# Kernel tuning notes

Measured on AMD Instinct MI355X. Metric: run time of the kernel, lower is better.

## Reference

```python
import jax, jax.numpy as jnp
import numpy as np

DIM = 768
NUM_HEADS = 12
HEAD_DIM = DIM // NUM_HEADS
SCALE = HEAD_DIM ** -0.5


def setup_inputs() -> dict:
    key = jax.random.key(0)
    k_x, k_qkv, k_proj, k_pb = jax.random.split(key, 4)
    B, N = 8, 1024
    x = jax.random.normal(k_x, (B, N, DIM), dtype=jnp.float32)
    # nn.Linear(dim, 3*dim, bias=False): weight [3*dim, dim]
    w_qkv = jax.random.normal(k_qkv, (3 * DIM, DIM), dtype=jnp.float32) * (DIM ** -0.5)
    # nn.Linear(dim, dim): weight [dim, dim], bias [dim]
    w_proj = jax.random.normal(k_proj, (DIM, DIM), dtype=jnp.float32) * (DIM ** -0.5)
    b_proj = jax.random.normal(k_pb, (DIM,), dtype=jnp.float32) * 0.01
    return {"x": x, "w_qkv": w_qkv, "w_proj": w_proj, "b_proj": b_proj}


def reference(x, w_qkv, w_proj, b_proj):
    B, N, C = x.shape
    H, D = NUM_HEADS, HEAD_DIM
    # qkv: [B, N, 3C] -> [3, B, H, N, D]
    qkv = jnp.einsum('bnc,oc->bno', x, w_qkv)
    qkv = qkv.reshape(B, N, 3, H, D).transpose(2, 0, 3, 1, 4)
    q, k, v = qkv[0], qkv[1], qkv[2]
    # scores in float32 (module explicitly casts to float)
    attn = jnp.einsum('bhnd,bhmd->bhnm', q.astype(jnp.float32), k.astype(jnp.float32)) * SCALE
    attn = jax.nn.softmax(attn, axis=-1)
    attn = jnp.where(jnp.isnan(attn), 0.0, attn)  # masked_fill nan -> 0
    out = jnp.einsum('bhnm,bhmd->bhnd', attn, v.astype(jnp.float32))
    out = out.transpose(0, 2, 1, 3).reshape(B, N, C)
    out = jnp.einsum('bnc,oc->bno', out, w_proj) + b_proj
    return out
```

## Files before the change

### kernel.cpp

```cpp
#include <hip/hip_runtime.h>

typedef _Float16 half8 __attribute__((ext_vector_type(8)));
typedef _Float16 half4 __attribute__((ext_vector_type(4)));
typedef float f32x4 __attribute__((ext_vector_type(4)));

#define NHEAD 12
#define HDIM  64
#define SEQ   1024
#define CDIM  768
#define O3    2304
#define MTOK  8192

__device__ __forceinline__ void load_lds16(const void* g, void* l) {
  __builtin_amdgcn_global_load_lds(
      (const __attribute__((address_space(1))) unsigned int*)g,
      (__attribute__((address_space(3))) unsigned int*)l, 16, 0, 0);
}

__global__ __launch_bounds__(256) void cast_f2h(const float* __restrict__ in,
                                                _Float16* __restrict__ out) {
  size_t i = ((size_t)blockIdx.x * 256 + threadIdx.x) * 4;
  float4 v = *reinterpret_cast<const float4*>(in + i);
  half4 h;
  h[0] = (_Float16)v.x; h[1] = (_Float16)v.y; h[2] = (_Float16)v.z; h[3] = (_Float16)v.w;
  *reinterpret_cast<half4*>(out + i) = h;
}

__global__ __launch_bounds__(256, 4) void qkv_gemm(const _Float16* __restrict__ A,
                                                   const _Float16* __restrict__ Bw,
                                                   _Float16* __restrict__ Qh,
                                                   _Float16* __restrict__ Kh,
                                                   _Float16* __restrict__ VT) {
  __shared__ _Float16 As0[128 * 32], Bs0[128 * 32];
  __shared__ _Float16 As1[128 * 32], Bs1[128 * 32];
  const int tid  = threadIdx.x;
  const int lane = tid & 63;
  const int wv   = tid >> 6;
  const int wm   = wv >> 1;
  const int wn   = wv & 1;
  const int fr   = lane & 15;
  const int kg   = lane >> 4;

  const int lin = blockIdx.y * gridDim.x + blockIdx.x;
  const int k   = lin & 7;
  const int j   = lin >> 3;
  const int n0  = (j >> 3) * 128;
  const int m0  = (k * 8 + (j & 7)) * 128;

  f32x4 acc[4][4];
#pragma unroll
  for (int i = 0; i < 4; ++i)
#pragma unroll
    for (int j2 = 0; j2 < 4; ++j2) acc[i][j2] = (f32x4){0.f, 0.f, 0.f, 0.f};

  auto stage = [&](_Float16* Ad, _Float16* Bd, int kt) {
#pragma unroll
    for (int r = 0; r < 2; ++r) {
      const int c = r * 256 + tid;
      const int row = c >> 2, cc = c & 3;
      load_lds16(A + (size_t)(m0 + row) * CDIM + kt + ((cc ^ (row & 3)) * 8), Ad + c * 8);
    }
#pragma unroll
    for (int r = 0; r < 2; ++r) {
      const int c = r * 256 + tid;
      const int row = c >> 2, cc = c & 3;
      load_lds16(Bw + (size_t)(n0 + row) * CDIM + kt + ((cc ^ (row & 3)) * 8), Bd + c * 8);
    }
  };

  auto compute = [&](const _Float16* As, const _Float16* Bs) {
    half8 a[4], b[4];
#pragma unroll
    for (int i = 0; i < 4; ++i) {
      const int row = wm * 64 + i * 16 + fr;
      a[i] = *reinterpret_cast<const half8*>(&As[row * 32 + ((kg ^ (row & 3)) * 8)]);
    }
#pragma unroll
    for (int j2 = 0; j2 < 4; ++j2) {
      const int row = wn * 64 + j2 * 16 + fr;
      b[j2] = *reinterpret_cast<const half8*>(&Bs[row * 32 + ((kg ^ (row & 3)) * 8)]);
    }
#pragma unroll
    for (int i = 0; i < 4; ++i)
#pragma unroll
      for (int j2 = 0; j2 < 4; ++j2)
        acc[i][j2] = __builtin_amdgcn_mfma_f32_16x16x32_f16(a[i], b[j2], acc[i][j2], 0, 0, 0);
  };

  stage(As0, Bs0, 0);
  __syncthreads();
  for (int it = 0; it < 12; ++it) {
    const int kt = it * 64;
    stage(As1, Bs1, kt + 32);
    compute(As0, Bs0);
    __syncthreads();
    if (kt + 64 < CDIM) stage(As0, Bs0, kt + 64);
    compute(As1, Bs1);
    __syncthreads();
  }

  const float QSCALE = 0.125f * 1.44269504088896f;
  const int t     = n0 / CDIM;
  const int hbase = n0 - t * CDIM;
#pragma unroll
  for (int i = 0; i < 4; ++i) {
    const int mrow = m0 + wm * 64 + i * 16 + kg * 4;
#pragma unroll
    for (int j2 = 0; j2 < 4; ++j2) {
      const int hd = hbase + wn * 64 + j2 * 16 + fr;
      const int h  = hd >> 6, d = hd & 63;
#pragma unroll
      for (int r = 0; r < 4; ++r) {
        const int m  = mrow + r;
        const int bb = m >> 10, nn = m & 1023;
        const float v = acc[i][j2][r];
        if (t == 0)
          Qh[(((size_t)(bb * NHEAD + h)) << 16) + (nn << 6) + d] = (_Float16)(v * QSCALE);
        else if (t == 1)
          Kh[(((size_t)(bb * NHEAD + h)) << 16) + (nn << 6) + d] = (_Float16)v;
        else
          VT[(((size_t)(bb * NHEAD + h)) << 16) + (d << 10) + nn] = (_Float16)v;
      }
    }
  }
}

__global__ __launch_bounds__(512) void attn_kernel(const _Float16* __restrict__ Qh,
                                                   const _Float16* __restrict__ Kh,
                                                   const _Float16* __restrict__ VT,
                                                   _Float16* __restrict__ AO) {
  __shared__ _Float16 Ks0[64 * 64], Vs0[64 * 64];
  __shared__ _Float16 Ks1[64 * 64], Vs1[64 * 64];
  __shared__ _Float16 Ps[8 * 16 * 64];
  const int tid  = threadIdx.x;
  const int lane = tid & 63;
  const int w    = tid >> 6;
  const int fr   = lane & 15;
  const int kg   = lane >> 4;
  const int kh   = kg * 8;
  const int bh   = blockIdx.x;
  const int qt   = blockIdx.y;
  const int q0   = qt * 128 + w * 16;
  const size_t qkbase = (size_t)bh * SEQ * HDIM;
  char* const psw = (char*)&Ps[w * 16 * 64];

  half8 qb[2];
#pragma unroll
  for (int ks = 0; ks < 2; ++ks)
    qb[ks] = *reinterpret_cast<const half8*>(
        &Qh[qkbase + (size_t)(q0 + fr) * HDIM + ks * 32 + kh]);

  f32x4 O[4];
  float mrun = -__builtin_inff();
  float lrun = 0.f;
#pragma unroll
  for (int fd = 0; fd < 4; ++fd) O[fd] = (f32x4){0.f, 0.f, 0.f, 0.f};

  auto stageKV = [&](_Float16* Kd, _Float16* Vd, int kt) {
    const int c = tid;
    const int row = c >> 3, cc = c & 7;
    load_lds16(&Kh[qkbase + (size_t)(kt + row) * HDIM + ((cc ^ (row & 7)) * 8)], Kd + c * 8);
    load_lds16(&VT[(size_t)bh * HDIM * SEQ + (size_t)row * SEQ + kt + ((cc ^ (row & 7)) * 8)],
               Vd + c * 8);
  };

  auto computeKV = [&](const _Float16* Ksrc, const _Float16* Vsrc) {
    f32x4 st[4];
#pragma unroll
    for (int fc = 0; fc < 4; ++fc) st[fc] = (f32x4){0.f, 0.f, 0.f, 0.f};
#pragma unroll
    for (int ks = 0; ks < 2; ++ks) {
#pragma unroll
      for (int fc = 0; fc < 4; ++fc) {
        const int row = fc * 16 + fr;
        const int colh = ks * 32 + kh;
        half8 ka = *reinterpret_cast<const half8*>(
            &Ksrc[row * 64 + (((colh >> 3) ^ (row & 7)) << 3)]);
        st[fc] = __builtin_amdgcn_mfma_f32_16x16x32_f16(ka, qb[ks], st[fc], 0, 0, 0);
      }
    }

    float mx = st[0][0];
#pragma unroll
    for (int fc = 0; fc < 4; ++fc)
#pragma unroll
      for (int r = 0; r < 4; ++r) mx = fmaxf(mx, st[fc][r]);
    mx = fmaxf(mx, __shfl_xor(mx, 16));
    mx = fmaxf(mx, __shfl_xor(mx, 32));

    if (!__all(mx - mrun <= 8.f)) {
      const float mnew = fmaxf(mrun, mx);
      const float corr = exp2f(mrun - mnew);
      mrun = mnew;
      lrun *= corr;
#pragma unroll
      for (int r = 0; r < 4; ++r) {
        const float c4 = __shfl(corr, kg * 4 + r);
#pragma unroll
        for (int fd = 0; fd < 4; ++fd) O[fd][r] *= c4;
      }
    }

    float rs = 0.f;
#pragma unroll
    for (int fc = 0; fc < 4; ++fc)
#pragma unroll
      for (int r = 0; r < 4; ++r) {
        const float p = exp2f(st[fc][r] - mrun);
        st[fc][r] = p;
        rs += p;
      }
    rs += __shfl_xor(rs, 16);
    rs += __shfl_xor(rs, 32);
    lrun += rs;

#pragma unroll
    for (int fc = 0; fc < 4; ++fc) {
      half4 pk;
      pk[0] = (_Float16)st[fc][0];
      pk[1] = (_Float16)st[fc][1];
      pk[2] = (_Float16)st[fc][2];
      pk[3] = (_Float16)st[fc][3];
      const int slot = (fc * 2 + (kg >> 1)) ^ (fr & 7);
      *reinterpret_cast<half4*>(psw + fr * 128 + slot * 16 + (kg & 1) * 8) = pk;
    }

#pragma unroll
    for (int ks = 0; ks < 2; ++ks) {
      const int rslot = (ks * 4 + kg) ^ (fr & 7);
      half8 pa = *reinterpret_cast<half8*>(psw + fr * 128 + rslot * 16);
#pragma unroll
      for (int fd = 0; fd < 4; ++fd) {
        const int row = fd * 16 + fr;
        const int colh = ks * 32 + kh;
        half8 vb = *reinterpret_cast<const half8*>(
            &Vsrc[row * 64 + (((colh >> 3) ^ (row & 7)) << 3)]);
        O[fd] = __builtin_amdgcn_mfma_f32_16x16x32_f16(pa, vb, O[fd], 0, 0, 0);
      }
    }
  };

  stageKV(Ks0, Vs0, 0);
  __syncthreads();
  for (int it = 0; it < 8; ++it) {
    const int kt = it * 128;
    stageKV(Ks1, Vs1, kt + 64);
    computeKV(Ks0, Vs0);
    __syncthreads();
    if (kt + 128 < SEQ) stageKV(Ks0, Vs0, kt + 128);
    computeKV(Ks1, Vs1);
    __syncthreads();
  }

  const int b = bh / NHEAD, h = bh % NHEAD;
  const float linv = 1.0f / lrun;
#pragma unroll
  for (int r = 0; r < 4; ++r) {
    const float lq = __shfl(linv, kg * 4 + r);
    const int n = q0 + kg * 4 + r;
#pragma unroll
    for (int fd = 0; fd < 4; ++fd)
      AO[((size_t)b * SEQ + n) * CDIM + h * HDIM + fd * 16 + fr] =
          (_Float16)(O[fd][r] * lq);
  }
}

__global__ __launch_bounds__(256, 4) void proj_gemm(const _Float16* __restrict__ A,
                                                    const _Float16* __restrict__ Bw,
                                                    const float* __restrict__ bias,
                                                    float* __restrict__ Out) {
  __shared__ _Float16 As0[128 * 32], Bs0[128 * 32];
  __shared__ _Float16 As1[128 * 32], Bs1[128 * 32];
  const int tid  = threadIdx.x;
  const int lane = tid & 63;
  const int wv   = tid >> 6;
  const int wm   = wv >> 1;
  const int wn   = wv & 1;
  const int fr   = lane & 15;
  const int kg   = lane >> 4;

  const int lin = blockIdx.y * gridDim.x + blockIdx.x;
  const int k   = lin & 7;
  const int j   = lin >> 3;
  const int n0  = (j >> 3) * 128;
  const int m0  = (k * 8 + (j & 7)) * 128;

  f32x4 acc[4][4];
#pragma unroll
  for (int i = 0; i < 4; ++i)
#pragma unroll
    for (int j2 = 0; j2 < 4; ++j2) acc[i][j2] = (f32x4){0.f, 0.f, 0.f, 0.f};

  auto stage = [&](_Float16* Ad, _Float16* Bd, int kt) {
#pragma unroll
    for (int r = 0; r < 2; ++r) {
      const int c = r * 256 + tid;
      const int row = c >> 2, cc = c & 3;
      load_lds16(A + (size_t)(m0 + row) * CDIM + kt + ((cc ^ (row & 3)) * 8), Ad + c * 8);
    }
#pragma unroll
    for (int r = 0; r < 2; ++r) {
      const int c = r * 256 + tid;
      const int row = c >> 2, cc = c & 3;
      load_lds16(Bw + (size_t)(n0 + row) * CDIM + kt + ((cc ^ (row & 3)) * 8), Bd + c * 8);
    }
  };

  auto compute = [&](const _Float16* As, const _Float16* Bs) {
    half8 a[4], b[4];
#pragma unroll
    for (int i = 0; i < 4; ++i) {
      const int row = wm * 64 + i * 16 + fr;
      a[i] = *reinterpret_cast<const half8*>(&As[row * 32 + ((kg ^ (row & 3)) * 8)]);
    }
#pragma unroll
    for (int j2 = 0; j2 < 4; ++j2) {
      const int row = wn * 64 + j2 * 16 + fr;
      b[j2] = *reinterpret_cast<const half8*>(&Bs[row * 32 + ((kg ^ (row & 3)) * 8)]);
    }
#pragma unroll
    for (int i = 0; i < 4; ++i)
#pragma unroll
      for (int j2 = 0; j2 < 4; ++j2)
        acc[i][j2] = __builtin_amdgcn_mfma_f32_16x16x32_f16(a[i], b[j2], acc[i][j2], 0, 0, 0);
  };

  stage(As0, Bs0, 0);
  __syncthreads();
  for (int it = 0; it < 12; ++it) {
    const int kt = it * 64;
    stage(As1, Bs1, kt + 32);
    compute(As0, Bs0);
    __syncthreads();
    if (kt + 64 < CDIM) stage(As0, Bs0, kt + 64);
    compute(As1, Bs1);
    __syncthreads();
  }

#pragma unroll
  for (int i = 0; i < 4; ++i) {
    const int mrow = m0 + wm * 64 + i * 16 + kg * 4;
#pragma unroll
    for (int j2 = 0; j2 < 4; ++j2) {
      const int ocol = n0 + wn * 64 + j2 * 16 + fr;
      const float bv = bias[ocol];
#pragma unroll
      for (int r = 0; r < 4; ++r)
        Out[(size_t)(mrow + r) * CDIM + ocol] = acc[i][j2][r] + bv;
    }
  }
}

extern "C" void kernel_launch(void* const* d_in, const int* in_sizes, int n_in,
                              void* d_out, int out_size, void* d_ws, size_t ws_size,
                              hipStream_t stream) {
  const float* x     = (const float*)d_in[0];
  const float* wqkv  = (const float*)d_in[1];
  const float* wproj = (const float*)d_in[2];
  const float* bproj = (const float*)d_in[3];
  float* out = (float*)d_out;

  char* ws = (char*)d_ws;
  _Float16* x_h     = (_Float16*)(ws);
  _Float16* wqkv_h  = (_Float16*)(ws + 12582912);
  _Float16* wproj_h = (_Float16*)(ws + 16121856);
  _Float16* Qh      = (_Float16*)(ws + 17301504);
  _Float16* Kh      = (_Float16*)(ws + 29884416);
  _Float16* VT      = (_Float16*)(ws + 42467328);
  _Float16* AOh     = (_Float16*)(ws + 55050240);

  cast_f2h<<<6291456 / 1024, 256, 0, stream>>>(x, x_h);
  cast_f2h<<<1769472 / 1024, 256, 0, stream>>>(wqkv, wqkv_h);
  cast_f2h<<<589824 / 1024, 256, 0, stream>>>(wproj, wproj_h);

  qkv_gemm<<<dim3(O3 / 128, MTOK / 128), 256, 0, stream>>>(x_h, wqkv_h, Qh, Kh, VT);
  attn_kernel<<<dim3(96, 8), 512, 0, stream>>>(Qh, Kh, VT, AOh);
  proj_gemm<<<dim3(CDIM / 128, MTOK / 128), 256, 0, stream>>>(AOh, wproj_h, bproj, out);
}
```

Measured before the change: 139.1 us.

## Use 4-stage LDS ring with vmcnt waits and stronger swizzle in GEMMs

The QKV and projection GEMMs move from a double buffer with two __syncthreads per 64-wide K step to a 4-slot LDS ring. Loads run two 32-wide K tiles ahead, with one barrier per tile and explicit s_waitcnt vmcnt counts, so global-to-LDS loads overlap MFMA compute. The LDS XOR swizzle also folds in (row>>2)&3 to cut bank conflicts on fragment reads. LDS per block doubles to 64KB and the minimum-occupancy hint of 4 blocks is dropped, which may lower occupancy. The hand-set vmcnt values are fragile if the compiler reorders or adds memory ops.

```diff
diff --git a/kernel.cpp b/kernel.cpp
--- a/kernel.cpp
+++ b/kernel.cpp
@@ -26,13 +26,13 @@
   *reinterpret_cast<half4*>(out + i) = h;
 }
 
-__global__ __launch_bounds__(256, 4) void qkv_gemm(const _Float16* __restrict__ A,
-                                                   const _Float16* __restrict__ Bw,
-                                                   _Float16* __restrict__ Qh,
-                                                   _Float16* __restrict__ Kh,
-                                                   _Float16* __restrict__ VT) {
-  __shared__ _Float16 As0[128 * 32], Bs0[128 * 32];
-  __shared__ _Float16 As1[128 * 32], Bs1[128 * 32];
+__global__ __launch_bounds__(256) void qkv_gemm(const _Float16* __restrict__ A,
+                                                const _Float16* __restrict__ Bw,
+                                                _Float16* __restrict__ Qh,
+                                                _Float16* __restrict__ Kh,
+                                                _Float16* __restrict__ VT) {
+  __shared__ _Float16 AsAll[4][128 * 32];
+  __shared__ _Float16 BsAll[4][128 * 32];
   const int tid  = threadIdx.x;
   const int lane = tid & 63;
   const int wv   = tid >> 6;
@@ -40,6 +40,7 @@
   const int wn   = wv & 1;
   const int fr   = lane & 15;
   const int kg   = lane >> 4;
+  const int kswz = kg ^ (fr & 3) ^ ((fr >> 2) & 3);
 
   const int lin = blockIdx.y * gridDim.x + blockIdx.x;
   const int k   = lin & 7;
@@ -53,18 +54,22 @@
 #pragma unroll
     for (int j2 = 0; j2 < 4; ++j2) acc[i][j2] = (f32x4){0.f, 0.f, 0.f, 0.f};
 
-  auto stage = [&](_Float16* Ad, _Float16* Bd, int kt) {
+  auto stage = [&](int slot, int kt) {
+    _Float16* Ad = AsAll[slot];
+    _Float16* Bd = BsAll[slot];
 #pragma unroll
     for (int r = 0; r < 2; ++r) {
       const int c = r * 256 + tid;
       const int row = c >> 2, cc = c & 3;
-      load_lds16(A + (size_t)(m0 + row) * CDIM + kt + ((cc ^ (row & 3)) * 8), Ad + c * 8);
+      const int g = cc ^ (row & 3) ^ ((row >> 2) & 3);
+      load_lds16(A + (size_t)(m0 + row) * CDIM + kt + g * 8, Ad + c * 8);
     }
 #pragma unroll
     for (int r = 0; r < 2; ++r) {
       const int c = r * 256 + tid;
       const int row = c >> 2, cc = c & 3;
-      load_lds16(Bw + (size_t)(n0 + row) * CDIM + kt + ((cc ^ (row & 3)) * 8), Bd + c * 8);
+      const int g = cc ^ (row & 3) ^ ((row >> 2) & 3);
+      load_lds16(Bw + (size_t)(n0 + row) * CDIM + kt + g * 8, Bd + c * 8);
     }
   };
 
@@ -73,12 +78,12 @@
 #pragma unroll
     for (int i = 0; i < 4; ++i) {
       const int row = wm * 64 + i * 16 + fr;
-      a[i] = *reinterpret_cast<const half8*>(&As[row * 32 + ((kg ^ (row & 3)) * 8)]);
+      a[i] = *reinterpret_cast<const half8*>(&As[row * 32 + kswz * 8]);
     }
 #pragma unroll
     for (int j2 = 0; j2 < 4; ++j2) {
       const int row = wn * 64 + j2 * 16 + fr;
-      b[j2] = *reinterpret_cast<const half8*>(&Bs[row * 32 + ((kg ^ (row & 3)) * 8)]);
+      b[j2] = *reinterpret_cast<const half8*>(&Bs[row * 32 + kswz * 8]);
     }
 #pragma unroll
     for (int i = 0; i < 4; ++i)
@@ -87,16 +92,20 @@
         acc[i][j2] = __builtin_amdgcn_mfma_f32_16x16x32_f16(a[i], b[j2], acc[i][j2], 0, 0, 0);
   };
 
-  stage(As0, Bs0, 0);
-  __syncthreads();
-  for (int it = 0; it < 12; ++it) {
-    const int kt = it * 64;
-    stage(As1, Bs1, kt + 32);
-    compute(As0, Bs0);
-    __syncthreads();
-    if (kt + 64 < CDIM) stage(As0, Bs0, kt + 64);
-    compute(As1, Bs1);
-    __syncthreads();
+  stage(0, 0);
+  stage(1, 32);
+  for (int it = 0; it < 24; ++it) {
+    if (it + 2 < 24) {
+      stage((it + 2) & 3, (it + 2) * 32);
+      asm volatile("s_waitcnt vmcnt(8)" ::: "memory");
+    } else if (it + 1 < 24) {
+      asm volatile("s_waitcnt vmcnt(4)" ::: "memory");
+    } else {
+      asm volatile("s_waitcnt vmcnt(0)" ::: "memory");
+    }
+    __builtin_amdgcn_s_barrier();
+    __builtin_amdgcn_sched_barrier(0);
+    compute(AsAll[it & 3], BsAll[it & 3]);
   }
 
   const float QSCALE = 0.125f * 1.44269504088896f;
@@ -265,12 +274,12 @@
   }
 }
 
-__global__ __launch_bounds__(256, 4) void proj_gemm(const _Float16* __restrict__ A,
-                                                    const _Float16* __restrict__ Bw,
-                                                    const float* __restrict__ bias,
-                                                    float* __restrict__ Out) {
-  __shared__ _Float16 As0[128 * 32], Bs0[128 * 32];
-  __shared__ _Float16 As1[128 * 32], Bs1[128 * 32];
+__global__ __launch_bounds__(256) void proj_gemm(const _Float16* __restrict__ A,
+                                                 const _Float16* __restrict__ Bw,
+                                                 const float* __restrict__ bias,
+                                                 float* __restrict__ Out) {
+  __shared__ _Float16 AsAll[4][128 * 32];
+  __shared__ _Float16 BsAll[4][128 * 32];
   const int tid  = threadIdx.x;
   const int lane = tid & 63;
   const int wv   = tid >> 6;
@@ -278,6 +287,7 @@
   const int wn   = wv & 1;
   const int fr   = lane & 15;
   const int kg   = lane >> 4;
+  const int kswz = kg ^ (fr & 3) ^ ((fr >> 2) & 3);
 
   const int lin = blockIdx.y * gridDim.x + blockIdx.x;
   const int k   = lin & 7;
@@ -291,18 +301,22 @@
 #pragma unroll
     for (int j2 = 0; j2 < 4; ++j2) acc[i][j2] = (f32x4){0.f, 0.f, 0.f, 0.f};
 
-  auto stage = [&](_Float16* Ad, _Float16* Bd, int kt) {
+  auto stage = [&](int slot, int kt) {
+    _Float16* Ad = AsAll[slot];
+    _Float16* Bd = BsAll[slot];
 #pragma unroll
     for (int r = 0; r < 2; ++r) {
       const int c = r * 256 + tid;
       const int row = c >> 2, cc = c & 3;
-      load_lds16(A + (size_t)(m0 + row) * CDIM + kt + ((cc ^ (row & 3)) * 8), Ad + c * 8);
+      const int g = cc ^ (row & 3) ^ ((row >> 2) & 3);
+      load_lds16(A + (size_t)(m0 + row) * CDIM + kt + g * 8, Ad + c * 8);
     }
 #pragma unroll
     for (int r = 0; r < 2; ++r) {
       const int c = r * 256 + tid;
       const int row = c >> 2, cc = c & 3;
-      load_lds16(Bw + (size_t)(n0 + row) * CDIM + kt + ((cc ^ (row & 3)) * 8), Bd + c * 8);
+      const int g = cc ^ (row & 3) ^ ((row >> 2) & 3);
+      load_lds16(Bw + (size_t)(n0 + row) * CDIM + kt + g * 8, Bd + c * 8);
     }
   };
 
@@ -311,12 +325,12 @@
 #pragma unroll
     for (int i = 0; i < 4; ++i) {
       const int row = wm * 64 + i * 16 + fr;
-      a[i] = *reinterpret_cast<const half8*>(&As[row * 32 + ((kg ^ (row & 3)) * 8)]);
+      a[i] = *reinterpret_cast<const half8*>(&As[row * 32 + kswz * 8]);
     }
 #pragma unroll
     for (int j2 = 0; j2 < 4; ++j2) {
       const int row = wn * 64 + j2 * 16 + fr;
-      b[j2] = *reinterpret_cast<const half8*>(&Bs[row * 32 + ((kg ^ (row & 3)) * 8)]);
+      b[j2] = *reinterpret_cast<const half8*>(&Bs[row * 32 + kswz * 8]);
     }
 #pragma unroll
     for (int i = 0; i < 4; ++i)
@@ -325,16 +339,20 @@
         acc[i][j2] = __builtin_amdgcn_mfma_f32_16x16x32_f16(a[i], b[j2], acc[i][j2], 0, 0, 0);
   };
 
-  stage(As0, Bs0, 0);
-  __syncthreads();
-  for (int it = 0; it < 12; ++it) {
-    const int kt = it * 64;
-    stage(As1, Bs1, kt + 32);
-    compute(As0, Bs0);
-    __syncthreads();
-    if (kt + 64 < CDIM) stage(As0, Bs0, kt + 64);
-    compute(As1, Bs1);
-    __syncthreads();
+  stage(0, 0);
+  stage(1, 32);
+  for (int it = 0; it < 24; ++it) {
+    if (it + 2 < 24) {
+      stage((it + 2) & 3, (it + 2) * 32);
+      asm volatile("s_waitcnt vmcnt(8)" ::: "memory");
+    } else if (it + 1 < 24) {
+      asm volatile("s_waitcnt vmcnt(4)" ::: "memory");
+    } else {
+      asm volatile("s_waitcnt vmcnt(0)" ::: "memory");
+    }
+    __builtin_amdgcn_s_barrier();
+    __builtin_amdgcn_sched_barrier(0);
+    compute(AsAll[it & 3], BsAll[it & 3]);
   }
 
 #pragma unroll
```

New measurement: 145.1 us. 4.3% more time.

## Deepen GEMM LDS pipeline to four stages with explicit waitcnt and barriers

Applied to the files above, without the earlier changes.

Both the QKV and projection GEMMs now use a four-buffer LDS ring, two tiles each 64 wide in K, filled by async global-to-LDS loads issued up to two half-steps ahead. Fine-grained vmcnt waits, raw s_barrier, sched_barrier fences and setprio around the MFMA block replace the older double buffer with __syncthreads, which drained all loads at every step. The LDS swizzle changes from row&3 to (row>>1)&3 to cut bank conflicts, and the occupancy hint of 4 is dropped. LDS per block doubles to 64KB, which may lower occupancy, and the hand-counted vmcnt values must be exact or results will be wrong.

```diff
diff --git a/kernel.cpp b/kernel.cpp
--- a/kernel.cpp
+++ b/kernel.cpp
@@ -10,6 +10,7 @@
 #define CDIM  768
 #define O3    2304
 #define MTOK  8192
+#define NT    12
 
 __device__ __forceinline__ void load_lds16(const void* g, void* l) {
   __builtin_amdgcn_global_load_lds(
@@ -26,26 +27,98 @@
   *reinterpret_cast<half4*>(out + i) = h;
 }
 
-__global__ __launch_bounds__(256, 4) void qkv_gemm(const _Float16* __restrict__ A,
-                                                   const _Float16* __restrict__ Bw,
-                                                   _Float16* __restrict__ Qh,
-                                                   _Float16* __restrict__ Kh,
-                                                   _Float16* __restrict__ VT) {
-  __shared__ _Float16 As0[128 * 32], Bs0[128 * 32];
-  __shared__ _Float16 As1[128 * 32], Bs1[128 * 32];
-  const int tid  = threadIdx.x;
-  const int lane = tid & 63;
-  const int wv   = tid >> 6;
-  const int wm   = wv >> 1;
-  const int wn   = wv & 1;
-  const int fr   = lane & 15;
+
+#define GEMM_IDS                                           \
+  const int tid  = threadIdx.x;                            \
+  const int lane = tid & 63;                               \
+  const int wv   = tid >> 6;                               \
+  const int wm   = wv >> 1;                                \
+  const int wn   = wv & 1;                                 \
+  const int fr   = lane & 15;                              \
   const int kg   = lane >> 4;
 
+#define GEMM_STAGE(Abase, Bbase, tb, kk, kcol)             \
+  {                                                        \
+    _Float16* Ad = &Ab[tb][kk][0];                         \
+    _Float16* Bd = &Bb[tb][kk][0];                         \
+    _Unroll_ for (int r = 0; r < 2; ++r) {                 \
+      const int c = r * 256 + tid;                         \
+      const int row = c >> 2, cc = c & 3;                  \
+      const int off = (cc ^ ((row >> 1) & 3)) * 8;         \
+      load_lds16(Abase + (size_t)(m0 + row) * CDIM + (kcol) + off, Ad + c * 8); \
+    }                                                      \
+    _Unroll_ for (int r = 0; r < 2; ++r) {                 \
+      const int c = r * 256 + tid;                         \
+      const int row = c >> 2, cc = c & 3;                  \
+      const int off = (cc ^ ((row >> 1) & 3)) * 8;         \
+      load_lds16(Bbase + (size_t)(n0 + row) * CDIM + (kcol) + off, Bd + c * 8); \
+    }                                                      \
+  }
+
+#define GEMM_READS(tb, kk)                                 \
+  _Unroll_ for (int i = 0; i < 4; ++i) {                   \
+    const int row = wm * 64 + i * 16 + fr;                 \
+    a[i] = *reinterpret_cast<const half8*>(                \
+        &Ab[tb][kk][row * 32 + ((kg ^ ((row >> 1) & 3)) * 8)]); \
+  }                                                        \
+  _Unroll_ for (int j2 = 0; j2 < 4; ++j2) {                \
+    const int row = wn * 64 + j2 * 16 + fr;                \
+    b[j2] = *reinterpret_cast<const half8*>(               \
+        &Bb[tb][kk][row * 32 + ((kg ^ ((row >> 1) & 3)) * 8)]); \
+  }
+
+#define GEMM_MFMA                                          \
+  __builtin_amdgcn_s_setprio(1);                           \
+  _Unroll_ for (int i = 0; i < 4; ++i)                     \
+    _Unroll_ for (int j2 = 0; j2 < 4; ++j2)                \
+      acc[i][j2] = __builtin_amdgcn_mfma_f32_16x16x32_f16(a[i], b[j2], acc[i][j2], 0, 0, 0); \
+  __builtin_amdgcn_s_setprio(0);
+
+#define SB __builtin_amdgcn_sched_barrier(0)
+#define BAR __builtin_amdgcn_s_barrier()
+#define VMC(n) asm volatile("s_waitcnt vmcnt(" #n ")" ::: "memory")
+#define _Unroll_ _Pragma("unroll")
+
+#define GEMM_MAINLOOP(Abase, Bbase)                        \
+  GEMM_STAGE(Abase, Bbase, 0, 0, 0);                       \
+  GEMM_STAGE(Abase, Bbase, 0, 1, 32);                      \
+  GEMM_STAGE(Abase, Bbase, 1, 0, 64);                      \
+  VMC(8); BAR; SB;                                         \
+  for (int t = 0; t < NT; ++t) {                           \
+    const int tb = t & 1;                                  \
+    half8 a[4], b[4];                                      \
+                                       \
+    GEMM_READS(tb, 0);                                     \
+    if (t + 1 < NT) GEMM_STAGE(Abase, Bbase, tb ^ 1, 1, (t + 1) * 64 + 32); \
+    SB;                                                    \
+    if (t < NT - 1) { VMC(8); } else { VMC(0); }           \
+    BAR; SB;                                               \
+    GEMM_MFMA; SB; BAR; SB;                                \
+                                       \
+    GEMM_READS(tb, 1);                                     \
+    if (t + 2 < NT) GEMM_STAGE(Abase, Bbase, tb, 0, (t + 2) * 64); \
+    SB;                                                    \
+    if (t < NT - 2) { VMC(8); }                            \
+    else if (t == NT - 2) { VMC(4); }                      \
+    else { VMC(0); }                                       \
+    BAR; SB;                                               \
+    GEMM_MFMA; SB; BAR; SB;                                \
+  }
+
+__global__ __launch_bounds__(256) void qkv_gemm(const _Float16* __restrict__ A,
+                                                const _Float16* __restrict__ Bw,
+                                                _Float16* __restrict__ Qh,
+                                                _Float16* __restrict__ Kh,
+                                                _Float16* __restrict__ VT) {
+  __shared__ _Float16 Ab[2][2][128 * 32];
+  __shared__ _Float16 Bb[2][2][128 * 32];
+  GEMM_IDS;
+
   const int lin = blockIdx.y * gridDim.x + blockIdx.x;
-  const int k   = lin & 7;
-  const int j   = lin >> 3;
-  const int n0  = (j >> 3) * 128;
-  const int m0  = (k * 8 + (j & 7)) * 128;
+  const int xk  = lin & 7;
+  const int xj  = lin >> 3;
+  const int n0  = (xj >> 3) * 128;
+  const int m0  = (xk * 8 + (xj & 7)) * 128;
 
   f32x4 acc[4][4];
 #pragma unroll
@@ -53,55 +126,11 @@
 #pragma unroll
     for (int j2 = 0; j2 < 4; ++j2) acc[i][j2] = (f32x4){0.f, 0.f, 0.f, 0.f};
 
-  auto stage = [&](_Float16* Ad, _Float16* Bd, int kt) {
-#pragma unroll
-    for (int r = 0; r < 2; ++r) {
-      const int c = r * 256 + tid;
-      const int row = c >> 2, cc = c & 3;
-      load_lds16(A + (size_t)(m0 + row) * CDIM + kt + ((cc ^ (row & 3)) * 8), Ad + c * 8);
-    }
-#pragma unroll
-    for (int r = 0; r < 2; ++r) {
-      const int c = r * 256 + tid;
-      const int row = c >> 2, cc = c & 3;
-      load_lds16(Bw + (size_t)(n0 + row) * CDIM + kt + ((cc ^ (row & 3)) * 8), Bd + c * 8);
-    }
-  };
-
-  auto compute = [&](const _Float16* As, const _Float16* Bs) {
-    half8 a[4], b[4];
-#pragma unroll
-    for (int i = 0; i < 4; ++i) {
-      const int row = wm * 64 + i * 16 + fr;
-      a[i] = *reinterpret_cast<const half8*>(&As[row * 32 + ((kg ^ (row & 3)) * 8)]);
-    }
-#pragma unroll
-    for (int j2 = 0; j2 < 4; ++j2) {
-      const int row = wn * 64 + j2 * 16 + fr;
-      b[j2] = *reinterpret_cast<const half8*>(&Bs[row * 32 + ((kg ^ (row & 3)) * 8)]);
-    }
-#pragma unroll
-    for (int i = 0; i < 4; ++i)
-#pragma unroll
-      for (int j2 = 0; j2 < 4; ++j2)
-        acc[i][j2] = __builtin_amdgcn_mfma_f32_16x16x32_f16(a[i], b[j2], acc[i][j2], 0, 0, 0);
-  };
-
-  stage(As0, Bs0, 0);
-  __syncthreads();
-  for (int it = 0; it < 12; ++it) {
-    const int kt = it * 64;
-    stage(As1, Bs1, kt + 32);
-    compute(As0, Bs0);
-    __syncthreads();
-    if (kt + 64 < CDIM) stage(As0, Bs0, kt + 64);
-    compute(As1, Bs1);
-    __syncthreads();
-  }
+  GEMM_MAINLOOP(A, Bw);
 
   const float QSCALE = 0.125f * 1.44269504088896f;
-  const int t     = n0 / CDIM;
-  const int hbase = n0 - t * CDIM;
+  const int t0    = n0 / CDIM;
+  const int hbase = n0 - t0 * CDIM;
 #pragma unroll
   for (int i = 0; i < 4; ++i) {
     const int mrow = m0 + wm * 64 + i * 16 + kg * 4;
@@ -114,9 +143,9 @@
         const int m  = mrow + r;
         const int bb = m >> 10, nn = m & 1023;
         const float v = acc[i][j2][r];
-        if (t == 0)
+        if (t0 == 0)
           Qh[(((size_t)(bb * NHEAD + h)) << 16) + (nn << 6) + d] = (_Float16)(v * QSCALE);
-        else if (t == 1)
+        else if (t0 == 1)
           Kh[(((size_t)(bb * NHEAD + h)) << 16) + (nn << 6) + d] = (_Float16)v;
         else
           VT[(((size_t)(bb * NHEAD + h)) << 16) + (d << 10) + nn] = (_Float16)v;
@@ -265,25 +294,19 @@
   }
 }
 
-__global__ __launch_bounds__(256, 4) void proj_gemm(const _Float16* __restrict__ A,
-                                                    const _Float16* __restrict__ Bw,
-                                                    const float* __restrict__ bias,
-                                                    float* __restrict__ Out) {
-  __shared__ _Float16 As0[128 * 32], Bs0[128 * 32];
-  __shared__ _Float16 As1[128 * 32], Bs1[128 * 32];
-  const int tid  = threadIdx.x;
-  const int lane = tid & 63;
-  const int wv   = tid >> 6;
-  const int wm   = wv >> 1;
-  const int wn   = wv & 1;
-  const int fr   = lane & 15;
-  const int kg   = lane >> 4;
+__global__ __launch_bounds__(256) void proj_gemm(const _Float16* __restrict__ A,
+                                                 const _Float16* __restrict__ Bw,
+                                                 const float* __restrict__ bias,
+                                                 float* __restrict__ Out) {
+  __shared__ _Float16 Ab[2][2][128 * 32];
+  __shared__ _Float16 Bb[2][2][128 * 32];
+  GEMM_IDS;
 
   const int lin = blockIdx.y * gridDim.x + blockIdx.x;
-  const int k   = lin & 7;
-  const int j   = lin >> 3;
-  const int n0  = (j >> 3) * 128;
-  const int m0  = (k * 8 + (j & 7)) * 128;
+  const int xk  = lin & 7;
+  const int xj  = lin >> 3;
+  const int n0  = (xj >> 3) * 128;
+  const int m0  = (xk * 8 + (xj & 7)) * 128;
 
   f32x4 acc[4][4];
 #pragma unroll
@@ -291,51 +314,7 @@
 #pragma unroll
     for (int j2 = 0; j2 < 4; ++j2) acc[i][j2] = (f32x4){0.f, 0.f, 0.f, 0.f};
 
-  auto stage = [&](_Float16* Ad, _Float16* Bd, int kt) {
-#pragma unroll
-    for (int r = 0; r < 2; ++r) {
-      const int c = r * 256 + tid;
-      const int row = c >> 2, cc = c & 3;
-      load_lds16(A + (size_t)(m0 + row) * CDIM + kt + ((cc ^ (row & 3)) * 8), Ad + c * 8);
-    }
-#pragma unroll
-    for (int r = 0; r < 2; ++r) {
-      const int c = r * 256 + tid;
-      const int row = c >> 2, cc = c & 3;
-      load_lds16(Bw + (size_t)(n0 + row) * CDIM + kt + ((cc ^ (row & 3)) * 8), Bd + c * 8);
-    }
-  };
-
-  auto compute = [&](const _Float16* As, const _Float16* Bs) {
-    half8 a[4], b[4];
-#pragma unroll
-    for (int i = 0; i < 4; ++i) {
-      const int row = wm * 64 + i * 16 + fr;
-      a[i] = *reinterpret_cast<const half8*>(&As[row * 32 + ((kg ^ (row & 3)) * 8)]);
-    }
-#pragma unroll
-    for (int j2 = 0; j2 < 4; ++j2) {
-      const int row = wn * 64 + j2 * 16 + fr;
-      b[j2] = *reinterpret_cast<const half8*>(&Bs[row * 32 + ((kg ^ (row & 3)) * 8)]);
-    }
-#pragma unroll
-    for (int i = 0; i < 4; ++i)
-#pragma unroll
-      for (int j2 = 0; j2 < 4; ++j2)
-        acc[i][j2] = __builtin_amdgcn_mfma_f32_16x16x32_f16(a[i], b[j2], acc[i][j2], 0, 0, 0);
-  };
-
-  stage(As0, Bs0, 0);
-  __syncthreads();
-  for (int it = 0; it < 12; ++it) {
-    const int kt = it * 64;
-    stage(As1, Bs1, kt + 32);
-    compute(As0, Bs0);
-    __syncthreads();
-    if (kt + 64 < CDIM) stage(As0, Bs0, kt + 64);
-    compute(As1, Bs1);
-    __syncthreads();
-  }
+  GEMM_MAINLOOP(A, Bw);
 
 #pragma unroll
   for (int i = 0; i < 4; ++i) {
```

New measurement: 141.0 us. Within noise of the previous version (+1.4%).
